# Performance work log

Measured on AMD Instinct MI355X. Metric: run time of the kernel, lower is better.

Reference implementation:

```python
import jax, jax.numpy as jnp
import numpy as np

N = 100_000          # number of nodes
E = 3_200_000        # number of edges (avg degree 32)
IN_CH = 128
OUT_CH = 128


def setup_inputs() -> dict:
    key = jax.random.key(0)
    k1, k2, k3, k4 = jax.random.split(key, 4)
    x = jax.random.normal(k1, (N, IN_CH), dtype=jnp.float32)
    edge_index = jax.random.randint(k2, (2, E), 0, N, dtype=jnp.int32)
    # torch nn.Linear weights have shape [out_features, in_features]
    W_theta = jax.random.normal(k3, (OUT_CH, IN_CH), dtype=jnp.float32) / np.sqrt(IN_CH).astype(np.float32)
    W_phi = jax.random.normal(k4, (OUT_CH, OUT_CH), dtype=jnp.float32) / np.sqrt(OUT_CH).astype(np.float32)
    return {"x": x, "edge_index": edge_index, "W_theta": W_theta, "W_phi": W_phi}


def reference(x, edge_index, W_theta, W_phi):
    row, col = edge_index[0], edge_index[1]
    rel_pos = x[row] - x[col]                       # [E, in]
    rel_t = rel_pos @ W_theta.T                     # [E, out]
    aggr = jax.ops.segment_max(rel_t, row, num_segments=N)  # [N, out], -inf for empty segments
    # torch_scatter.scatter_max leaves empty segments at 0
    aggr = jnp.where(jnp.isneginf(aggr), jnp.zeros((), dtype=aggr.dtype), aggr)
    return aggr @ W_phi.T                           # [N, out]
```

## Files before the change

### kernel.cpp

```cpp
#include <hip/hip_runtime.h>
#include <stdint.h>

#define N_NODES 100000
#define N_EDGES 3200000
#define CH 128
#define NBUK 391
#define CAP 8704
#define SPLIT_BLOCKS 1563

typedef __bf16 bf16x8 __attribute__((ext_vector_type(8)));
typedef float  floatx4 __attribute__((ext_vector_type(4)));

__device__ __forceinline__ unsigned short f2bf_bits(float f) {
    unsigned u = __float_as_uint(f);
    u += 0x7FFFu + ((u >> 16) & 1u);
    return (unsigned short)(u >> 16);
}

__device__ __forceinline__ unsigned short enc16(unsigned short b) {
    return b ^ ((b & 0x8000u) ? 0xFFFFu : 0x8000u);
}

__device__ __forceinline__ unsigned pkminu(unsigned a, unsigned b) {
    unsigned d;
    asm("v_pk_min_u16 %0, %1, %2" : "=v"(d) : "v"(a), "v"(b));
    return d;
}

__device__ __forceinline__ unsigned dec2(unsigned k) {
    unsigned lo = k & 0xFFFFu;
    unsigned hi = k >> 16;
    lo ^= (lo & 0x8000u) ? 0x8000u : 0xFFFFu;
    hi ^= (hi & 0x8000u) ? 0x8000u : 0xFFFFu;
    return lo | (hi << 16);
}

__device__ __forceinline__ bf16x8 pack8(floatx4 f0, floatx4 f1) {
    bf16x8 r;
    r[0] = (__bf16)f0[0]; r[1] = (__bf16)f0[1]; r[2] = (__bf16)f0[2]; r[3] = (__bf16)f0[3];
    r[4] = (__bf16)f1[0]; r[5] = (__bf16)f1[1]; r[6] = (__bf16)f1[2]; r[7] = (__bf16)f1[3];
    return r;
}

__global__ void k_setup(const float* __restrict__ Wt, const float* __restrict__ Wp,
                        unsigned short* __restrict__ wb, int* __restrict__ cursor) {
    int bid = blockIdx.x, t = threadIdx.x;
    if (bid < 128) {
        int i = bid * 256 + t;
        float v = (i < 16384) ? Wt[i] : Wp[i - 16384];
        wb[i] = f2bf_bits(v);
    } else {
        for (int i = t; i < NBUK; i += 256) cursor[i] = i * CAP;
    }
}

__global__ void k_split(const int* __restrict__ row, const int* __restrict__ col,
                        int* __restrict__ cursor, unsigned* __restrict__ pairs) {
    __shared__ int h[NBUK];
    __shared__ int basebuf[NBUK];
    int bid = blockIdx.x, t = threadIdx.x;
    for (int i = t; i < NBUK; i += 256) h[i] = 0;
    __syncthreads();
    int e0 = bid * 2048;
    int4 r[2];
    bool v[2];
#pragma unroll
    for (int j = 0; j < 2; j++) {
        int idx = e0 + j * 1024 + t * 4;
        v[j] = idx < N_EDGES;
        if (v[j]) {
            r[j] = *(const int4*)(row + idx);
            atomicAdd(&h[r[j].x >> 8], 1);
            atomicAdd(&h[r[j].y >> 8], 1);
            atomicAdd(&h[r[j].z >> 8], 1);
            atomicAdd(&h[r[j].w >> 8], 1);
        }
    }
    __syncthreads();
    for (int i = t; i < NBUK; i += 256) {
        int c = h[i];
        basebuf[i] = c ? atomicAdd(&cursor[i], c) : 0;
        h[i] = 0;
    }
    __syncthreads();
#pragma unroll
    for (int j = 0; j < 2; j++) {
        if (v[j]) {
            int idx = e0 + j * 1024 + t * 4;
            int4 c = *(const int4*)(col + idx);
            int b, p;
            b = r[j].x >> 8; p = basebuf[b] + atomicAdd(&h[b], 1);
            if (p < (b + 1) * CAP) pairs[p] = ((unsigned)(r[j].x & 255) << 17) | (unsigned)c.x;
            b = r[j].y >> 8; p = basebuf[b] + atomicAdd(&h[b], 1);
            if (p < (b + 1) * CAP) pairs[p] = ((unsigned)(r[j].y & 255) << 17) | (unsigned)c.y;
            b = r[j].z >> 8; p = basebuf[b] + atomicAdd(&h[b], 1);
            if (p < (b + 1) * CAP) pairs[p] = ((unsigned)(r[j].z & 255) << 17) | (unsigned)c.z;
            b = r[j].w >> 8; p = basebuf[b] + atomicAdd(&h[b], 1);
            if (p < (b + 1) * CAP) pairs[p] = ((unsigned)(r[j].w & 255) << 17) | (unsigned)c.w;
        }
    }
}

__global__ void k_build_gemmy(unsigned* __restrict__ pairs, const int* __restrict__ cursor,
                              int* __restrict__ deg, int* __restrict__ offs,
                              const float* __restrict__ x,
                              const unsigned short* __restrict__ wb,
                              unsigned short* __restrict__ yt) {
    int bid = blockIdx.x, t = threadIdx.x;
    if (bid < NBUK) {
        __shared__ int hist[256];
        __shared__ int sc[256];
        __shared__ int cur[256];
        __shared__ int lcsr[CAP];
        int b = bid;
        int s0 = b * CAP;
        int cnt = cursor[b] - s0;
        if (cnt > CAP) cnt = CAP;
        if (t < 256) hist[t] = 0;
        __syncthreads();
        for (int i = t; i < cnt; i += 1024) {
            unsigned p = pairs[s0 + i];
            atomicAdd(&hist[p >> 17], 1);
        }
        __syncthreads();
        int d = 0;
        if (t < 256) { d = hist[t]; sc[t] = d; }
        __syncthreads();
        for (int off = 1; off < 256; off <<= 1) {
            int vv = 0;
            if (t < 256 && t >= off) vv = sc[t - off];
            __syncthreads();
            if (t < 256) sc[t] += vv;
            __syncthreads();
        }
        if (t < 256) {
            int excl = sc[t] - d;
            int node = b * 256 + t;
            if (node < N_NODES) {
                deg[node] = d;
                offs[node] = s0 + excl;
            }
            cur[t] = excl;
        }
        __syncthreads();
        for (int i = t; i < cnt; i += 1024) {
            unsigned p = pairs[s0 + i];
            int pos = atomicAdd(&cur[p >> 17], 1);
            lcsr[pos] = (int)(p & 0x1FFFFu);
        }
        __syncthreads();
        int* csr = (int*)pairs;
        for (int i = t; i < cnt; i += 1024) csr[s0 + i] = lcsr[i];
    } else {
        int w = (bid - NBUK) * 16 + (t >> 6);
        int lane = t & 63;
        int row0 = w * 16;
        if (row0 >= N_NODES) return;
        int m = lane & 15, quad = lane >> 4;

        bf16x8 a[4];
        const floatx4* xp = (const floatx4*)(x + (size_t)(row0 + m) * CH + quad * 8);
#pragma unroll
        for (int ks = 0; ks < 4; ks++) a[ks] = pack8(xp[ks * 8], xp[ks * 8 + 1]);

        for (int nt = 0; nt < 8; nt++) {
            const bf16x8* wp = (const bf16x8*)(wb + (size_t)(nt * 16 + m) * CH + quad * 8);
            floatx4 acc = {0.f, 0.f, 0.f, 0.f};
#pragma unroll
            for (int ks = 0; ks < 4; ks++)
                acc = __builtin_amdgcn_mfma_f32_16x16x32_bf16(a[ks], wp[ks * 4], acc, 0, 0, 0);
#pragma unroll
            for (int r = 0; r < 4; r++) {
                int orow = row0 + quad * 4 + r;
                yt[(size_t)orow * CH + nt * 16 + m] = enc16(f2bf_bits(acc[r]));
            }
        }
    }
}

#define PKA(v)                        \
    do {                              \
        m0 = pkminu(m0, (v).x);       \
        m1 = pkminu(m1, (v).y);       \
        m2 = pkminu(m2, (v).z);       \
        m3 = pkminu(m3, (v).w);       \
    } while (0)

__global__ void k_minaggr_out(const uint4* __restrict__ yt, const int* __restrict__ offs,
                              const int* __restrict__ deg, const int* __restrict__ csr,
                              const unsigned short* __restrict__ wb,
                              float* __restrict__ out) {
    __shared__ unsigned short atile[16 * 136];
    int t = threadIdx.x;
    int wave = t >> 6, lane = t & 63;
    int q = lane >> 4, s = lane & 15;
    int nl = wave * 4 + q;
    int n = blockIdx.x * 16 + nl;

    int i = offs[n];
    int len = deg[n];
    int end = i + len;

    unsigned m0 = ~0u, m1 = ~0u, m2 = ~0u, m3 = ~0u;

    for (; i + 8 <= end; i += 8) {
        int c0 = csr[i + 0];
        int c1 = csr[i + 1];
        int c2 = csr[i + 2];
        int c3 = csr[i + 3];
        int c4 = csr[i + 4];
        int c5 = csr[i + 5];
        int c6 = csr[i + 6];
        int c7 = csr[i + 7];
        uint4 v0 = yt[(size_t)c0 * 16 + s];
        uint4 v1 = yt[(size_t)c1 * 16 + s];
        uint4 v2 = yt[(size_t)c2 * 16 + s];
        uint4 v3 = yt[(size_t)c3 * 16 + s];
        uint4 v4 = yt[(size_t)c4 * 16 + s];
        uint4 v5 = yt[(size_t)c5 * 16 + s];
        uint4 v6 = yt[(size_t)c6 * 16 + s];
        uint4 v7 = yt[(size_t)c7 * 16 + s];
        PKA(v0); PKA(v1); PKA(v2); PKA(v3);
        PKA(v4); PKA(v5); PKA(v6); PKA(v7);
    }
    for (; i < end; i++) {
        int c = csr[i];
        uint4 v = yt[(size_t)c * 16 + s];
        PKA(v);
    }

    uint4 outv = {0u, 0u, 0u, 0u};
    if (len > 0) {
        unsigned d0 = dec2(m0), d1 = dec2(m1), d2 = dec2(m2), d3 = dec2(m3);
        uint4 se = yt[(size_t)n * 16 + s];
        unsigned s0 = dec2(se.x), s1 = dec2(se.y), s2 = dec2(se.z), s3 = dec2(se.w);
        outv.x = (unsigned)f2bf_bits(__uint_as_float(s0 << 16) - __uint_as_float(d0 << 16)) |
                 ((unsigned)f2bf_bits(__uint_as_float(s0 & 0xFFFF0000u) -
                                      __uint_as_float(d0 & 0xFFFF0000u)) << 16);
        outv.y = (unsigned)f2bf_bits(__uint_as_float(s1 << 16) - __uint_as_float(d1 << 16)) |
                 ((unsigned)f2bf_bits(__uint_as_float(s1 & 0xFFFF0000u) -
                                      __uint_as_float(d1 & 0xFFFF0000u)) << 16);
        outv.z = (unsigned)f2bf_bits(__uint_as_float(s2 << 16) - __uint_as_float(d2 << 16)) |
                 ((unsigned)f2bf_bits(__uint_as_float(s2 & 0xFFFF0000u) -
                                      __uint_as_float(d2 & 0xFFFF0000u)) << 16);
        outv.w = (unsigned)f2bf_bits(__uint_as_float(s3 << 16) - __uint_as_float(d3 << 16)) |
                 ((unsigned)f2bf_bits(__uint_as_float(s3 & 0xFFFF0000u) -
                                      __uint_as_float(d3 & 0xFFFF0000u)) << 16);
    }
    *(uint4*)&atile[nl * 136 + s * 8] = outv;
    __syncthreads();

    int m = lane & 15, quad = lane >> 4;
    bf16x8 a[4];
#pragma unroll
    for (int ks = 0; ks < 4; ks++)
        a[ks] = *(const bf16x8*)&atile[m * 136 + ks * 32 + quad * 8];

#pragma unroll
    for (int ntl = 0; ntl < 2; ntl++) {
        int nt = wave * 2 + ntl;
        const bf16x8* wp = (const bf16x8*)(wb + (size_t)(nt * 16 + m) * CH + quad * 8);
        floatx4 acc = {0.f, 0.f, 0.f, 0.f};
#pragma unroll
        for (int ks = 0; ks < 4; ks++)
            acc = __builtin_amdgcn_mfma_f32_16x16x32_bf16(a[ks], wp[ks * 4], acc, 0, 0, 0);
#pragma unroll
        for (int r = 0; r < 4; r++)
            out[(size_t)(blockIdx.x * 16 + quad * 4 + r) * CH + nt * 16 + m] = acc[r];
    }
}

extern "C" void kernel_launch(void* const* d_in, const int* in_sizes, int n_in,
                              void* d_out, int out_size, void* d_ws, size_t ws_size,
                              hipStream_t stream) {
    const float* x   = (const float*)d_in[0];
    const int* edge  = (const int*)d_in[1];
    const float* Wt  = (const float*)d_in[2];
    const float* Wp  = (const float*)d_in[3];
    const int* row = edge;
    const int* col = edge + N_EDGES;
    float* out = (float*)d_out;

    char* ws = (char*)d_ws;
    int* deg    = (int*)ws;  ws += 400128;
    int* offs   = (int*)ws;  ws += 400128;
    int* cursor = (int*)ws;  ws += 2048;
    unsigned short* yt = (unsigned short*)ws; ws += 25600000;
    unsigned short* wb = (unsigned short*)ws; ws += 65536;
    unsigned* pairs = (unsigned*)ws; ws += (size_t)NBUK * CAP * 4;

    k_setup<<<129, 256, 0, stream>>>(Wt, Wp, wb, cursor);
    k_split<<<SPLIT_BLOCKS, 256, 0, stream>>>(row, col, cursor, pairs);
    k_build_gemmy<<<NBUK + 391, 1024, 0, stream>>>(pairs, cursor, deg, offs, x, wb, yt);
    k_minaggr_out<<<N_NODES / 16, 256, 0, stream>>>((const uint4*)yt, offs, deg,
                                                    (const int*)pairs, wb + 16384, out);
}
```

Measured before the change: 337.5 us.

## Split node GEMM across split and build kernels; enlarge per-block edge chunks

The per-node x·W_theta GEMM is now divided: the first half of the rows runs in extra blocks of the edge-bucketing kernel and the rest in the CSR-build kernel. This overlaps dense MFMA work with the atomic-heavy scatter phases. The split kernel also processes 8192 edges per block instead of 2048, cutting the number of global cursor atomics but lowering its block count and raising register use from holding 8 int4 rows per thread.

```diff
diff --git a/kernel.cpp b/kernel.cpp
--- a/kernel.cpp
+++ b/kernel.cpp
@@ -6,7 +6,8 @@
 #define CH 128
 #define NBUK 391
 #define CAP 8704
-#define SPLIT_BLOCKS 1563
+#define SPLIT_BLOCKS 391
+#define ROWS_A 50048
 
 typedef __bf16 bf16x8 __attribute__((ext_vector_type(8)));
 typedef float  floatx4 __attribute__((ext_vector_type(4)));
@@ -40,6 +41,29 @@
     r[0] = (__bf16)f0[0]; r[1] = (__bf16)f0[1]; r[2] = (__bf16)f0[2]; r[3] = (__bf16)f0[3];
     r[4] = (__bf16)f1[0]; r[5] = (__bf16)f1[1]; r[6] = (__bf16)f1[2]; r[7] = (__bf16)f1[3];
     return r;
+}
+
+__device__ __forceinline__ void gemm_tile(int row0, int lane, const float* __restrict__ x,
+                                          const unsigned short* __restrict__ wb,
+                                          unsigned short* __restrict__ yt) {
+    int m = lane & 15, quad = lane >> 4;
+    bf16x8 a[4];
+    const floatx4* xp = (const floatx4*)(x + (size_t)(row0 + m) * CH + quad * 8);
+#pragma unroll
+    for (int ks = 0; ks < 4; ks++) a[ks] = pack8(xp[ks * 8], xp[ks * 8 + 1]);
+
+    for (int nt = 0; nt < 8; nt++) {
+        const bf16x8* wp = (const bf16x8*)(wb + (size_t)(nt * 16 + m) * CH + quad * 8);
+        floatx4 acc = {0.f, 0.f, 0.f, 0.f};
+#pragma unroll
+        for (int ks = 0; ks < 4; ks++)
+            acc = __builtin_amdgcn_mfma_f32_16x16x32_bf16(a[ks], wp[ks * 4], acc, 0, 0, 0);
+#pragma unroll
+        for (int r = 0; r < 4; r++) {
+            int orow = row0 + quad * 4 + r;
+            yt[(size_t)orow * CH + nt * 16 + m] = enc16(f2bf_bits(acc[r]));
+        }
+    }
 }
 
 __global__ void k_setup(const float* __restrict__ Wt, const float* __restrict__ Wp,
@@ -54,64 +78,74 @@
     }
 }
 
-__global__ void k_split(const int* __restrict__ row, const int* __restrict__ col,
-                        int* __restrict__ cursor, unsigned* __restrict__ pairs) {
+__global__ void k_split_gemmyA(const int* __restrict__ row, const int* __restrict__ col,
+                               int* __restrict__ cursor, unsigned* __restrict__ pairs,
+                               const float* __restrict__ x,
+                               const unsigned short* __restrict__ wb,
+                               unsigned short* __restrict__ yt) {
     __shared__ int h[NBUK];
     __shared__ int basebuf[NBUK];
     int bid = blockIdx.x, t = threadIdx.x;
-    for (int i = t; i < NBUK; i += 256) h[i] = 0;
-    __syncthreads();
-    int e0 = bid * 2048;
-    int4 r[2];
-    bool v[2];
-#pragma unroll
-    for (int j = 0; j < 2; j++) {
-        int idx = e0 + j * 1024 + t * 4;
-        v[j] = idx < N_EDGES;
-        if (v[j]) {
-            r[j] = *(const int4*)(row + idx);
-            atomicAdd(&h[r[j].x >> 8], 1);
-            atomicAdd(&h[r[j].y >> 8], 1);
-            atomicAdd(&h[r[j].z >> 8], 1);
-            atomicAdd(&h[r[j].w >> 8], 1);
-        }
-    }
-    __syncthreads();
-    for (int i = t; i < NBUK; i += 256) {
-        int c = h[i];
-        basebuf[i] = c ? atomicAdd(&cursor[i], c) : 0;
-        h[i] = 0;
-    }
-    __syncthreads();
-#pragma unroll
-    for (int j = 0; j < 2; j++) {
-        if (v[j]) {
+    if (bid < SPLIT_BLOCKS) {
+        for (int i = t; i < NBUK; i += 256) h[i] = 0;
+        __syncthreads();
+        int e0 = bid * 8192;
+        int4 r[8];
+        bool v[8];
+#pragma unroll
+        for (int j = 0; j < 8; j++) {
             int idx = e0 + j * 1024 + t * 4;
-            int4 c = *(const int4*)(col + idx);
-            int b, p;
-            b = r[j].x >> 8; p = basebuf[b] + atomicAdd(&h[b], 1);
-            if (p < (b + 1) * CAP) pairs[p] = ((unsigned)(r[j].x & 255) << 17) | (unsigned)c.x;
-            b = r[j].y >> 8; p = basebuf[b] + atomicAdd(&h[b], 1);
-            if (p < (b + 1) * CAP) pairs[p] = ((unsigned)(r[j].y & 255) << 17) | (unsigned)c.y;
-            b = r[j].z >> 8; p = basebuf[b] + atomicAdd(&h[b], 1);
-            if (p < (b + 1) * CAP) pairs[p] = ((unsigned)(r[j].z & 255) << 17) | (unsigned)c.z;
-            b = r[j].w >> 8; p = basebuf[b] + atomicAdd(&h[b], 1);
-            if (p < (b + 1) * CAP) pairs[p] = ((unsigned)(r[j].w & 255) << 17) | (unsigned)c.w;
-        }
-    }
-}
-
-__global__ void k_build_gemmy(unsigned* __restrict__ pairs, const int* __restrict__ cursor,
-                              int* __restrict__ deg, int* __restrict__ offs,
-                              const float* __restrict__ x,
-                              const unsigned short* __restrict__ wb,
-                              unsigned short* __restrict__ yt) {
+            v[j] = idx < N_EDGES;
+            if (v[j]) {
+                r[j] = *(const int4*)(row + idx);
+                atomicAdd(&h[r[j].x >> 8], 1);
+                atomicAdd(&h[r[j].y >> 8], 1);
+                atomicAdd(&h[r[j].z >> 8], 1);
+                atomicAdd(&h[r[j].w >> 8], 1);
+            }
+        }
+        __syncthreads();
+        for (int i = t; i < NBUK; i += 256) {
+            int c = h[i];
+            basebuf[i] = c ? atomicAdd(&cursor[i], c) : 0;
+            h[i] = 0;
+        }
+        __syncthreads();
+#pragma unroll
+        for (int j = 0; j < 8; j++) {
+            if (v[j]) {
+                int idx = e0 + j * 1024 + t * 4;
+                int4 c = *(const int4*)(col + idx);
+                int b, p;
+                b = r[j].x >> 8; p = basebuf[b] + atomicAdd(&h[b], 1);
+                if (p < (b + 1) * CAP) pairs[p] = ((unsigned)(r[j].x & 255) << 17) | (unsigned)c.x;
+                b = r[j].y >> 8; p = basebuf[b] + atomicAdd(&h[b], 1);
+                if (p < (b + 1) * CAP) pairs[p] = ((unsigned)(r[j].y & 255) << 17) | (unsigned)c.y;
+                b = r[j].z >> 8; p = basebuf[b] + atomicAdd(&h[b], 1);
+                if (p < (b + 1) * CAP) pairs[p] = ((unsigned)(r[j].z & 255) << 17) | (unsigned)c.z;
+                b = r[j].w >> 8; p = basebuf[b] + atomicAdd(&h[b], 1);
+                if (p < (b + 1) * CAP) pairs[p] = ((unsigned)(r[j].w & 255) << 17) | (unsigned)c.w;
+            }
+        }
+    } else {
+        int wave = (bid - SPLIT_BLOCKS) * 4 + (t >> 6);
+        int row0 = wave * 16;
+        if (row0 >= ROWS_A) return;
+        gemm_tile(row0, t & 63, x, wb, yt);
+    }
+}
+
+__global__ void k_build_gemmyB(unsigned* __restrict__ pairs, const int* __restrict__ cursor,
+                               int* __restrict__ deg, int* __restrict__ offs,
+                               const float* __restrict__ x,
+                               const unsigned short* __restrict__ wb,
+                               unsigned short* __restrict__ yt) {
+    __shared__ int hist[256];
+    __shared__ int sc[256];
+    __shared__ int cur[256];
+    __shared__ int lcsr[CAP];
     int bid = blockIdx.x, t = threadIdx.x;
     if (bid < NBUK) {
-        __shared__ int hist[256];
-        __shared__ int sc[256];
-        __shared__ int cur[256];
-        __shared__ int lcsr[CAP];
         int b = bid;
         int s0 = b * CAP;
         int cnt = cursor[b] - s0;
@@ -152,29 +186,10 @@
         int* csr = (int*)pairs;
         for (int i = t; i < cnt; i += 1024) csr[s0 + i] = lcsr[i];
     } else {
-        int w = (bid - NBUK) * 16 + (t >> 6);
-        int lane = t & 63;
-        int row0 = w * 16;
+        int wg = (bid - NBUK) * 16 + (t >> 6);
+        int row0 = ROWS_A + wg * 16;
         if (row0 >= N_NODES) return;
-        int m = lane & 15, quad = lane >> 4;
-
-        bf16x8 a[4];
-        const floatx4* xp = (const floatx4*)(x + (size_t)(row0 + m) * CH + quad * 8);
-#pragma unroll
-        for (int ks = 0; ks < 4; ks++) a[ks] = pack8(xp[ks * 8], xp[ks * 8 + 1]);
-
-        for (int nt = 0; nt < 8; nt++) {
-            const bf16x8* wp = (const bf16x8*)(wb + (size_t)(nt * 16 + m) * CH + quad * 8);
-            floatx4 acc = {0.f, 0.f, 0.f, 0.f};
-#pragma unroll
-            for (int ks = 0; ks < 4; ks++)
-                acc = __builtin_amdgcn_mfma_f32_16x16x32_bf16(a[ks], wp[ks * 4], acc, 0, 0, 0);
-#pragma unroll
-            for (int r = 0; r < 4; r++) {
-                int orow = row0 + quad * 4 + r;
-                yt[(size_t)orow * CH + nt * 16 + m] = enc16(f2bf_bits(acc[r]));
-            }
-        }
+        gemm_tile(row0, t & 63, x, wb, yt);
     }
 }
 
@@ -290,8 +305,9 @@
     unsigned* pairs = (unsigned*)ws; ws += (size_t)NBUK * CAP * 4;
 
     k_setup<<<129, 256, 0, stream>>>(Wt, Wp, wb, cursor);
-    k_split<<<SPLIT_BLOCKS, 256, 0, stream>>>(row, col, cursor, pairs);
-    k_build_gemmy<<<NBUK + 391, 1024, 0, stream>>>(pairs, cursor, deg, offs, x, wb, yt);
+    k_split_gemmyA<<<SPLIT_BLOCKS + 782, 256, 0, stream>>>(row, col, cursor, pairs,
+                                                           x, wb, yt);
+    k_build_gemmyB<<<NBUK + 196, 1024, 0, stream>>>(pairs, cursor, deg, offs, x, wb, yt);
     k_minaggr_out<<<N_NODES / 16, 256, 0, stream>>>((const uint4*)yt, offs, deg,
                                                     (const int*)pairs, wb + 16384, out);
 }
```

Result: faster. 296.9 us (-12.0%).
